# Performance work log

Measured on AMD Instinct MI355X. Metric: run time of the kernel, lower is better.

Reference implementation:

```python
import jax, jax.numpy as jnp
import numpy as np

IGNORE_INDEX = -100
BETA = 0.1
B, T, H, V = 4, 512, 4096, 32000

def setup_inputs() -> dict:
    key = jax.random.key(0)
    ks = jax.random.split(key, 8)
    s = 1.0 / np.sqrt(H)
    return {
        "_input": jax.random.normal(ks[0], (B, T, H), jnp.float32),
        "weight": jax.random.normal(ks[1], (V, H), jnp.float32) * s,
        "bias": jax.random.normal(ks[2], (V,), jnp.float32) * 0.01,
        "target": jax.random.randint(ks[3], (B, T), 0, V, jnp.int64),
        "preference_labels": jax.random.bernoulli(ks[4], 0.5, (B,)),
        "ref_input": jax.random.normal(ks[5], (B, T, H), jnp.float32),
        "ref_weight": jax.random.normal(ks[6], (V, H), jnp.float32) * s,
        "ref_bias": jax.random.normal(ks[7], (V,), jnp.float32) * 0.01,
        "kl": jax.random.uniform(jax.random.fold_in(key, 9), (1,), jnp.float32),
    }

def _avg_log_prob(x, w, b, target):
    # logits: [B, T, V]
    logits = jnp.einsum("bth,vh->btv", x, w) + b
    lse = jax.nn.logsumexp(logits, axis=-1)            # [B, T]
    idx = jnp.clip(target, 0, None)[..., None]
    tgt_logit = jnp.take_along_axis(logits, idx, axis=-1)[..., 0]
    per_tok_logp = tgt_logit - lse                     # [B, T]
    mask = (target != IGNORE_INDEX).astype(per_tok_logp.dtype)
    denom = jnp.maximum(mask.sum(-1), 1.0)
    return (per_tok_logp * mask).sum(-1) / denom       # [B]

def reference(_input, weight, bias, target, preference_labels, ref_input, ref_weight, ref_bias, kl):
    avg_logp = _avg_log_prob(_input, weight, bias, target)
    ref_avg_logp = jax.lax.stop_gradient(_avg_log_prob(ref_input, ref_weight, ref_bias, target))
    logratios = avg_logp - ref_avg_logp                # [B]
    multiplier = jnp.where(preference_labels, 1.0, -1.0)
    losses = 1.0 - jax.nn.sigmoid(BETA * (logratios - kl[0]) * multiplier)
    return losses.sum() / target.shape[0]
```

## Files before the change

### kernel.cpp

```cpp
#include <hip/hip_runtime.h>
#include <hip/hip_bf16.h>
#include <stdint.h>

#define HD 4096
#define VD 32000
#define BT 2048
#define TT 512
#define IGNORE_IDX (-100)

#define BM 256
#define BN 256
#define BKT 64
#define KT (HD / BKT)
#define NB (VD / BN)
#define MB (BT / BM)
#define NWG2 (MB * NB * 2)

#define NCHUNK (VD / 64)

typedef __attribute__((ext_vector_type(8))) short short8;
typedef __attribute__((ext_vector_type(4))) float f32x4;

__device__ __forceinline__ uint16_t f2bf(float f) {
    uint32_t u = __float_as_uint(f);
    u += 0x7FFFu + ((u >> 16) & 1u);
    return (uint16_t)(u >> 16);
}

__device__ __forceinline__ void gload16(const void* g, void* l) {
    __builtin_amdgcn_global_load_lds(
        (const __attribute__((address_space(1))) void*)g,
        (__attribute__((address_space(3))) void*)l, 16, 0, 0);
}

#define SBAR __builtin_amdgcn_sched_barrier(0)

__global__ void convert_x(const float* __restrict__ x0, const float* __restrict__ x1,
                          uint16_t* __restrict__ xbf) {
    const int64_t n4 = (int64_t)BT * HD / 4;
    ushort4* o0 = (ushort4*)xbf;
    ushort4* o1 = (ushort4*)(xbf + (int64_t)BT * HD);
    for (int64_t i = blockIdx.x * (int64_t)blockDim.x + threadIdx.x; i < n4;
         i += (int64_t)gridDim.x * blockDim.x) {
        float4 a = ((const float4*)x0)[i];
        float4 b = ((const float4*)x1)[i];
        ushort4 ua, ub;
        ua.x = f2bf(a.x); ua.y = f2bf(a.y); ua.z = f2bf(a.z); ua.w = f2bf(a.w);
        ub.x = f2bf(b.x); ub.y = f2bf(b.y); ub.z = f2bf(b.z); ub.w = f2bf(b.w);
        o0[i] = ua;
        o1[i] = ub;
    }
}

__global__ void convert_w(const float* __restrict__ w0, const float* __restrict__ w1,
                          uint16_t* __restrict__ wbf) {
    const int64_t n4 = (int64_t)VD * HD / 4;
    ushort4* o0 = (ushort4*)wbf;
    ushort4* o1 = (ushort4*)(wbf + (int64_t)VD * HD);
    for (int64_t i = blockIdx.x * (int64_t)blockDim.x + threadIdx.x; i < n4;
         i += (int64_t)gridDim.x * blockDim.x) {
        float4 a = ((const float4*)w0)[i];
        float4 b = ((const float4*)w1)[i];
        ushort4 ua, ub;
        ua.x = f2bf(a.x); ua.y = f2bf(a.y); ua.z = f2bf(a.z); ua.w = f2bf(a.w);
        ub.x = f2bf(b.x); ub.y = f2bf(b.y); ub.z = f2bf(b.z); ub.w = f2bf(b.w);
        o0[i] = ua;
        o1[i] = ub;
    }
}

__device__ __forceinline__ void mfma16(
    const short8& a0k0, const short8& a0k1, const short8& a1k0, const short8& a1k1,
    const short8 (&bfr)[4][2], f32x4* acc0, f32x4* acc1)
{
    __builtin_amdgcn_s_setprio(1);
#pragma unroll
    for (int ni = 0; ni < 4; ++ni)
        acc0[ni] = __builtin_amdgcn_mfma_f32_16x16x32_bf16(a0k0, bfr[ni][0], acc0[ni], 0, 0, 0);
#pragma unroll
    for (int ni = 0; ni < 4; ++ni)
        acc1[ni] = __builtin_amdgcn_mfma_f32_16x16x32_bf16(a1k0, bfr[ni][0], acc1[ni], 0, 0, 0);
#pragma unroll
    for (int ni = 0; ni < 4; ++ni)
        acc0[ni] = __builtin_amdgcn_mfma_f32_16x16x32_bf16(a0k1, bfr[ni][1], acc0[ni], 0, 0, 0);
#pragma unroll
    for (int ni = 0; ni < 4; ++ni)
        acc1[ni] = __builtin_amdgcn_mfma_f32_16x16x32_bf16(a1k1, bfr[ni][1], acc1[ni], 0, 0, 0);
    __builtin_amdgcn_s_setprio(0);
}

template<int CUR>
__device__ __forceinline__ void tile_body(
    int t,
    const uint16_t* __restrict__ agp, const uint16_t* __restrict__ bgp,
    char* aLdst, char* bLdst,
    const char* pA0, const char* pA1, const char* pB0, const char* pB1,
    f32x4 (&acc)[8][4])
{
    constexpr int CB  = CUR * 32768;
    constexpr int NXB = (CUR ^ 1) * 32768;
    const bool more = (t + 1) < KT;
    const int ko = (t + 1) * BKT;

    short8 bfr[4][2];
    short8 af0k0, af0k1, af1k0, af1k1;

#define BARR do { SBAR; __builtin_amdgcn_s_barrier(); SBAR; } while (0)
#define LOAD_AF(mi0)                                                   \
    af0k0 = *(const short8*)(pA0 + (mi0) * 2048 + CB);                 \
    af0k1 = *(const short8*)(pA1 + (mi0) * 2048 + CB);                 \
    af1k0 = *(const short8*)(pA0 + ((mi0) + 1) * 2048 + CB);           \
    af1k1 = *(const short8*)(pA1 + ((mi0) + 1) * 2048 + CB);

#pragma unroll
    for (int ni = 0; ni < 4; ++ni) {
        bfr[ni][0] = *(const short8*)(pB0 + ni * 2048 + CB);
        bfr[ni][1] = *(const short8*)(pB1 + ni * 2048 + CB);
    }
    LOAD_AF(0);
    if (more) {
        gload16(bgp + (size_t)(0 * 32) * HD + ko, bLdst + NXB + 0 * 4096);
        gload16(bgp + (size_t)(1 * 32) * HD + ko, bLdst + NXB + 1 * 4096);
    }
    BARR;
    mfma16(af0k0, af0k1, af1k0, af1k1, bfr, acc[0], acc[1]);
    BARR;

    LOAD_AF(2);
    if (more) {
        gload16(bgp + (size_t)(2 * 32) * HD + ko, bLdst + NXB + 2 * 4096);
        gload16(bgp + (size_t)(3 * 32) * HD + ko, bLdst + NXB + 3 * 4096);
    }
    BARR;
    mfma16(af0k0, af0k1, af1k0, af1k1, bfr, acc[2], acc[3]);
    SBAR; asm volatile("s_waitcnt vmcnt(4)" ::: "memory"); SBAR;
    BARR;

    LOAD_AF(4);
    if (more) {
        gload16(agp + (size_t)(0 * 32) * HD + ko, aLdst + NXB + 0 * 4096);
        gload16(agp + (size_t)(1 * 32) * HD + ko, aLdst + NXB + 1 * 4096);
    }
    BARR;
    mfma16(af0k0, af0k1, af1k0, af1k1, bfr, acc[4], acc[5]);
    BARR;

    LOAD_AF(6);
    if (more) {
        gload16(agp + (size_t)(2 * 32) * HD + ko, aLdst + NXB + 2 * 4096);
        gload16(agp + (size_t)(3 * 32) * HD + ko, aLdst + NXB + 3 * 4096);
    }
    BARR;
    mfma16(af0k0, af0k1, af1k0, af1k1, bfr, acc[6], acc[7]);
    SBAR;
    if (more) { asm volatile("s_waitcnt vmcnt(2)" ::: "memory"); }
    else      { asm volatile("s_waitcnt vmcnt(0)" ::: "memory"); }
    SBAR;
    BARR;
#undef LOAD_AF
#undef BARR
}

__global__ __launch_bounds__(512, 2) void gemm_lse_bf(
    const uint16_t* __restrict__ xbf, const uint16_t* __restrict__ wbf,
    const float* __restrict__ b0, const float* __restrict__ b1,
    const int* __restrict__ target,
    float* __restrict__ partials, float* __restrict__ tgtlog)
{
    __shared__ uint16_t As[2 * BM * BKT];
    __shared__ uint16_t Bs[2 * BN * BKT];

    const int orig = blockIdx.x;
    const int wgid = (orig & 7) * (NWG2 / 8) + (orig >> 3);
    const int mb    = wgid & 7;
    const int rest  = wgid >> 3;
    const int nb    = rest % NB;
    const int model = rest / NB;

    const uint16_t* xb = xbf + (size_t)model * BT * HD;
    const uint16_t* wb = wbf + (size_t)model * VD * HD;
    const float* bias  = model ? b1 : b0;

    const int row0 = mb * BM;
    const int c0   = nb * BN;

    const int tid    = threadIdx.x;
    const int lane   = tid & 63;
    const int wid    = tid >> 6;
    const int wr     = wid >> 2;
    const int wc     = wid & 3;

    const int lane15 = lane & 15;
    const int kg     = lane >> 4;
    const int swz    = (lane & 7) << 4;

    const int srow8 = lane >> 3;
    const int slot  = (lane & 7) ^ srow8;
    const uint16_t* agp = xb + (size_t)(row0 + wr * 128 + wc * 8 + srow8) * HD + slot * 8;
    const int bq = wr * 2 + (wc & 1);
    const uint16_t* bgp = wb + (size_t)(c0 + (wc >> 1) * 128 + bq * 8 + srow8) * HD + slot * 8;
    char* aLdst = (char*)As + wr * 16384 + wc * 1024;
    char* bLdst = (char*)Bs + (wc >> 1) * 16384 + bq * 1024;

    const int arow_b = wr * 128 + lane15;
    const int brow_b = wc * 64 + lane15;
    const char* pA0 = (const char*)As + ((arow_b * 128 + 0  + kg * 16) ^ swz);
    const char* pA1 = (const char*)As + ((arow_b * 128 + 64 + kg * 16) ^ swz);
    const char* pB0 = (const char*)Bs + ((brow_b * 128 + 0  + kg * 16) ^ swz);
    const char* pB1 = (const char*)Bs + ((brow_b * 128 + 64 + kg * 16) ^ swz);

    f32x4 acc[8][4];
#pragma unroll
    for (int i = 0; i < 8; ++i)
#pragma unroll
        for (int j = 0; j < 4; ++j) acc[i][j] = (f32x4){0.f, 0.f, 0.f, 0.f};

#pragma unroll
    for (int j = 0; j < 4; ++j)
        gload16(bgp + (size_t)(j * 32) * HD, bLdst + j * 4096);
#pragma unroll
    for (int j = 0; j < 4; ++j)
        gload16(agp + (size_t)(j * 32) * HD, aLdst + j * 4096);
    SBAR; asm volatile("s_waitcnt vmcnt(0)" ::: "memory"); SBAR;
    __builtin_amdgcn_s_barrier();
    SBAR;

    for (int t2 = 0; t2 < KT; t2 += 2) {
        tile_body<0>(t2,     agp, bgp, aLdst, bLdst, pA0, pA1, pB0, pB1, acc);
        tile_body<1>(t2 + 1, agp, bgp, aLdst, bLdst, pA0, pA1, pB0, pB1, acc);
    }

    float bv4[4];
#pragma unroll
    for (int ni = 0; ni < 4; ++ni) bv4[ni] = bias[c0 + wc * 64 + ni * 16 + lane15];

#pragma unroll
    for (int mi = 0; mi < 8; ++mi) {
        const int grow_base = row0 + wr * 128 + mi * 16 + kg * 4;
#pragma unroll
        for (int j = 0; j < 4; ++j) {
            const int grow = grow_base + j;
            float v[4];
#pragma unroll
            for (int ni = 0; ni < 4; ++ni) v[ni] = acc[mi][ni][j] + bv4[ni];
            float m = fmaxf(fmaxf(v[0], v[1]), fmaxf(v[2], v[3]));
#pragma unroll
            for (int msk = 1; msk < 16; msk <<= 1)
                m = fmaxf(m, __shfl_xor(m, msk));
            float s = __expf(v[0] - m) + __expf(v[1] - m) +
                      __expf(v[2] - m) + __expf(v[3] - m);
#pragma unroll
            for (int msk = 1; msk < 16; msk <<= 1)
                s += __shfl_xor(s, msk);
            const int tg = target[grow];
#pragma unroll
            for (int ni = 0; ni < 4; ++ni) {
                const int gcol = c0 + wc * 64 + ni * 16 + lane15;
                if (tg == gcol) tgtlog[model * BT + grow] = v[ni];
            }
            if (lane15 == 0) {
                const size_t po = ((size_t)(model * BT + grow) * NCHUNK + nb * 4 + wc) * 2;
                partials[po]     = m;
                partials[po + 1] = s;
            }
        }
    }
}

__global__ __launch_bounds__(256) void gemm_lse_f32(
    const uint16_t* __restrict__ xbf,
    const float* __restrict__ w0, const float* __restrict__ b0,
    const float* __restrict__ w1, const float* __restrict__ b1,
    const int* __restrict__ target,
    float* __restrict__ partials, float* __restrict__ tgtlog)
{
    const int orig = blockIdx.x;
    const int wgid = (orig & 7) * 1000 + (orig >> 3);
    const int mb    = wgid & 7;
    const int rest  = wgid >> 3;
    const int chunk = rest % 500;
    const int model = rest / 500;

    const float* w    = model ? w1 : w0;
    const float* bias = model ? b1 : b0;
    const uint16_t* xb = xbf + (size_t)model * BT * HD;

    const int row0 = mb * 256;
    const int c0   = chunk * 64;

    const int tid  = threadIdx.x;
    const int lane = tid & 63;
    const int wid  = tid >> 6;

    __shared__ uint16_t As_[256 * 64];
    __shared__ uint16_t Bs_[64 * 64];

    f32x4 acc[4][4];
#pragma unroll
    for (int i = 0; i < 4; ++i)
#pragma unroll
        for (int j = 0; j < 4; ++j) acc[i][j] = (f32x4){0.f, 0.f, 0.f, 0.f};

    const int srow8 = lane >> 3;
    const int slot  = (lane & 7) ^ srow8;
    const uint16_t* agsrc = xb + (size_t)(row0 + wid * 64 + srow8) * HD + slot * 8;
    char* aldst = (char*)As_ + wid * 8192;

    const int ss   = tid & 7;
    const int srow = tid >> 3;
    const int swz_w = (srow & 7) << 4;
    const float* bptr = w + (size_t)(c0 + srow) * HD + ss * 8;

    const int lane15 = lane & 15;
    const int kg     = lane >> 4;
    const int swz_r  = (lane & 7) << 4;

    for (int kt = 0; kt < 64; ++kt) {
        const int kofs = kt * 64;
#pragma unroll
        for (int c = 0; c < 8; ++c)
            gload16(agsrc + (size_t)c * 8 * HD + kofs, aldst + c * 1024);
        {
            float4 bv[2][2];
#pragma unroll
            for (int r = 0; r < 2; ++r) {
                const float* p = bptr + (size_t)r * 32 * HD + kofs;
                bv[r][0] = *(const float4*)(p);
                bv[r][1] = *(const float4*)(p + 4);
            }
#pragma unroll
            for (int r = 0; r < 2; ++r) {
                const int row_l = srow + r * 32;
                float fv[8] = {bv[r][0].x, bv[r][0].y, bv[r][0].z, bv[r][0].w,
                               bv[r][1].x, bv[r][1].y, bv[r][1].z, bv[r][1].w};
                uint32_t pk[4];
#pragma unroll
                for (int e = 0; e < 4; ++e)
                    pk[e] = (uint32_t)f2bf(fv[2 * e]) | ((uint32_t)f2bf(fv[2 * e + 1]) << 16);
                const int off = (row_l * 128 + ss * 16) ^ swz_w;
                *(uint4*)((char*)Bs_ + off) = *(uint4*)pk;
            }
        }
        __syncthreads();
#pragma unroll
        for (int ks = 0; ks < 2; ++ks) {
            short8 af[4], bf[4];
#pragma unroll
            for (int mi = 0; mi < 4; ++mi) {
                const int arow = wid * 64 + mi * 16 + lane15;
                const int off = (arow * 128 + ks * 64 + kg * 16) ^ swz_r;
                af[mi] = *(const short8*)((const char*)As_ + off);
            }
#pragma unroll
            for (int ni = 0; ni < 4; ++ni) {
                const int brow = ni * 16 + lane15;
                const int off = (brow * 128 + ks * 64 + kg * 16) ^ swz_r;
                bf[ni] = *(const short8*)((const char*)Bs_ + off);
            }
#pragma unroll
            for (int mi = 0; mi < 4; ++mi)
#pragma unroll
                for (int ni = 0; ni < 4; ++ni)
                    acc[mi][ni] = __builtin_amdgcn_mfma_f32_16x16x32_bf16(
                        af[mi], bf[ni], acc[mi][ni], 0, 0, 0);
        }
        __syncthreads();
    }

    float bv4[4];
#pragma unroll
    for (int ni = 0; ni < 4; ++ni) bv4[ni] = bias[c0 + ni * 16 + lane15];

#pragma unroll
    for (int mi = 0; mi < 4; ++mi) {
        const int grow_base = row0 + wid * 64 + mi * 16 + kg * 4;
#pragma unroll
        for (int j = 0; j < 4; ++j) {
            const int grow = grow_base + j;
            float v[4];
#pragma unroll
            for (int ni = 0; ni < 4; ++ni) v[ni] = acc[mi][ni][j] + bv4[ni];
            float m = fmaxf(fmaxf(v[0], v[1]), fmaxf(v[2], v[3]));
#pragma unroll
            for (int msk = 1; msk < 16; msk <<= 1)
                m = fmaxf(m, __shfl_xor(m, msk));
            float s = __expf(v[0] - m) + __expf(v[1] - m) +
                      __expf(v[2] - m) + __expf(v[3] - m);
#pragma unroll
            for (int msk = 1; msk < 16; msk <<= 1)
                s += __shfl_xor(s, msk);
            const int tg = target[grow];
#pragma unroll
            for (int ni = 0; ni < 4; ++ni) {
                const int gcol = c0 + ni * 16 + lane15;
                if (tg == gcol) tgtlog[model * BT + grow] = v[ni];
            }
            if (lane15 == 0) {
                const size_t po = ((size_t)(model * BT + grow) * NCHUNK + chunk) * 2;
                partials[po]     = m;
                partials[po + 1] = s;
            }
        }
    }
}

__global__ void lse_reduce(const float* __restrict__ partials,
                           const float* __restrict__ tgtlog,
                           float* __restrict__ logp) {
    const int gw = blockIdx.x * (blockDim.x >> 6) + (threadIdx.x >> 6);
    if (gw >= 2 * BT) return;
    const int lane = threadIdx.x & 63;
    const float* p = partials + (size_t)gw * NCHUNK * 2;

    float m = -1e30f;
#pragma unroll
    for (int i = 0; i < 8; ++i) {
        const int c = lane + i * 64;
        if (c < NCHUNK) m = fmaxf(m, p[c * 2]);
    }
#pragma unroll
    for (int msk = 1; msk < 64; msk <<= 1) m = fmaxf(m, __shfl_xor(m, msk));
    float s = 0.f;
#pragma unroll
    for (int i = 0; i < 8; ++i) {
        const int c = lane + i * 64;
        if (c < NCHUNK) s += p[c * 2 + 1] * __expf(p[c * 2] - m);
    }
#pragma unroll
    for (int msk = 1; msk < 64; msk <<= 1) s += __shfl_xor(s, msk);
    if (lane == 0) {
        const float lse = m + __logf(s);
        logp[gw] = tgtlog[gw] - lse;
    }
}

__global__ void final_loss(const float* __restrict__ logp, const int* __restrict__ target,
                           const int* __restrict__ pref, const float* __restrict__ kl,
                           float* __restrict__ out) {
    const int t = threadIdx.x;
    const int lane = t & 63, wv = t >> 6;
    __shared__ float rp[4][8], rr[4][8], rm[4][8];
#pragma unroll
    for (int b = 0; b < 4; ++b) {
        const int idx = b * TT + t;
        const int tg = target[idx];
        const bool mk = (tg != IGNORE_IDX);
        float lp = mk ? logp[idx] : 0.f;
        float lr = mk ? logp[BT + idx] : 0.f;
        float mc = mk ? 1.f : 0.f;
        for (int off = 32; off; off >>= 1) {
            lp += __shfl_down(lp, off);
            lr += __shfl_down(lr, off);
            mc += __shfl_down(mc, off);
        }
        if (lane == 0) { rp[b][wv] = lp; rr[b][wv] = lr; rm[b][wv] = mc; }
    }
    __syncthreads();
    if (t == 0) {
        float loss = 0.f;
        for (int b = 0; b < 4; ++b) {
            float sp = 0.f, sr = 0.f, sm = 0.f;
            for (int i = 0; i < 8; ++i) { sp += rp[b][i]; sr += rr[b][i]; sm += rm[b][i]; }
            const float denom = fmaxf(sm, 1.f);
            const float lrb = (sp - sr) / denom;
            const float mult = pref[b] ? 1.f : -1.f;
            const float z = 0.1f * (lrb - kl[0]) * mult;
            loss += 1.f / (1.f + __expf(z));
        }
        out[0] = loss * 0.25f;
    }
}

extern "C" void kernel_launch(void* const* d_in, const int* in_sizes, int n_in,
                              void* d_out, int out_size, void* d_ws, size_t ws_size,
                              hipStream_t stream) {
    const float* x    = (const float*)d_in[0];
    const float* w0   = (const float*)d_in[1];
    const float* b0   = (const float*)d_in[2];
    const int*   tgt  = (const int*)d_in[3];
    const int*   pref = (const int*)d_in[4];
    const float* xr   = (const float*)d_in[5];
    const float* w1   = (const float*)d_in[6];
    const float* b1   = (const float*)d_in[7];
    const float* kl   = (const float*)d_in[8];
    float* out = (float*)d_out;

    const size_t xbf_b  = (size_t)2 * BT * HD * 2;
    const size_t part_b = (size_t)2 * BT * NCHUNK * 2 * 4;
    const size_t tl_b   = (size_t)2 * BT * 4;
    const size_t wbf_b  = (size_t)2 * VD * HD * 2;

    char* wp = (char*)d_ws;
    uint16_t* xbf     = (uint16_t*)wp;                 wp += xbf_b;
    float*    partials = (float*)wp;                   wp += part_b;
    float*    tgtlog   = (float*)wp;                   wp += tl_b;
    float*    logp     = (float*)wp;                   wp += tl_b;
    uint16_t* wbf      = (uint16_t*)wp;
    const bool use_wbf = ws_size >= (xbf_b + part_b + 2 * tl_b + wbf_b);

    hipLaunchKernelGGL(convert_x, dim3(1024), dim3(256), 0, stream, x, xr, xbf);
    if (use_wbf) {
        hipLaunchKernelGGL(convert_w, dim3(4096), dim3(256), 0, stream, w0, w1, wbf);
        hipLaunchKernelGGL(gemm_lse_bf, dim3(NWG2), dim3(512), 0, stream,
                           xbf, wbf, b0, b1, tgt, partials, tgtlog);
    } else {
        hipLaunchKernelGGL(gemm_lse_f32, dim3(8000), dim3(256), 0, stream,
                           xbf, w0, b0, w1, b1, tgt, partials, tgtlog);
    }
    hipLaunchKernelGGL(lse_reduce, dim3(2 * BT / 4), dim3(256), 0, stream,
                       partials, tgtlog, logp);
    hipLaunchKernelGGL(final_loss, dim3(1), dim3(512), 0, stream, logp, tgt, pref, kl, out);
}
```

Measured before the change: 1.291 ms.

## Switch bf16 GEMM to 32x32x16 MFMA with restructured LDS reads and prefetch

Replaces the 16x16x32 bf16 MFMA tiling with 32x32x16 MFMA instructions. Each wave now holds a 4x2 grid of 16-float accumulators, and LDS fragments are read per k-slice with a matching XOR swizzle. All eight next-tile global-to-LDS loads are issued at the start of the first phase, with one full vmcnt wait at the end of each tile. The aim is fewer MFMA and LDS read instructions per flop and fewer split waits. The cost is an epilogue with 32-lane shuffle reductions and a larger per-instruction accumulator footprint.

```diff
diff --git a/kernel.cpp b/kernel.cpp
--- a/kernel.cpp
+++ b/kernel.cpp
@@ -20,6 +20,7 @@
 
 typedef __attribute__((ext_vector_type(8))) short short8;
 typedef __attribute__((ext_vector_type(4))) float f32x4;
+typedef __attribute__((ext_vector_type(16))) float f32x16;
 
 __device__ __forceinline__ uint16_t f2bf(float f) {
     uint32_t u = __float_as_uint(f);
@@ -69,95 +70,64 @@
     }
 }
 
-__device__ __forceinline__ void mfma16(
-    const short8& a0k0, const short8& a0k1, const short8& a1k0, const short8& a1k1,
-    const short8 (&bfr)[4][2], f32x4* acc0, f32x4* acc1)
-{
-    __builtin_amdgcn_s_setprio(1);
-#pragma unroll
-    for (int ni = 0; ni < 4; ++ni)
-        acc0[ni] = __builtin_amdgcn_mfma_f32_16x16x32_bf16(a0k0, bfr[ni][0], acc0[ni], 0, 0, 0);
-#pragma unroll
-    for (int ni = 0; ni < 4; ++ni)
-        acc1[ni] = __builtin_amdgcn_mfma_f32_16x16x32_bf16(a1k0, bfr[ni][0], acc1[ni], 0, 0, 0);
-#pragma unroll
-    for (int ni = 0; ni < 4; ++ni)
-        acc0[ni] = __builtin_amdgcn_mfma_f32_16x16x32_bf16(a0k1, bfr[ni][1], acc0[ni], 0, 0, 0);
-#pragma unroll
-    for (int ni = 0; ni < 4; ++ni)
-        acc1[ni] = __builtin_amdgcn_mfma_f32_16x16x32_bf16(a1k1, bfr[ni][1], acc1[ni], 0, 0, 0);
-    __builtin_amdgcn_s_setprio(0);
-}
+#define MFMA32(a, b, c) __builtin_amdgcn_mfma_f32_32x32x16_bf16(a, b, c, 0, 0, 0)
 
 template<int CUR>
 __device__ __forceinline__ void tile_body(
     int t,
     const uint16_t* __restrict__ agp, const uint16_t* __restrict__ bgp,
     char* aLdst, char* bLdst,
-    const char* pA0, const char* pA1, const char* pB0, const char* pB1,
-    f32x4 (&acc)[8][4])
+    const char* pAk0, const char* pAk1, const char* pAk2, const char* pAk3,
+    const char* pBk0, const char* pBk1, const char* pBk2, const char* pBk3,
+    f32x16 (&acc)[4][2])
 {
     constexpr int CB  = CUR * 32768;
     constexpr int NXB = (CUR ^ 1) * 32768;
     const bool more = (t + 1) < KT;
     const int ko = (t + 1) * BKT;
 
-    short8 bfr[4][2];
-    short8 af0k0, af0k1, af1k0, af1k1;
-
 #define BARR do { SBAR; __builtin_amdgcn_s_barrier(); SBAR; } while (0)
-#define LOAD_AF(mi0)                                                   \
-    af0k0 = *(const short8*)(pA0 + (mi0) * 2048 + CB);                 \
-    af0k1 = *(const short8*)(pA1 + (mi0) * 2048 + CB);                 \
-    af1k0 = *(const short8*)(pA0 + ((mi0) + 1) * 2048 + CB);           \
-    af1k1 = *(const short8*)(pA1 + ((mi0) + 1) * 2048 + CB);
-
-#pragma unroll
-    for (int ni = 0; ni < 4; ++ni) {
-        bfr[ni][0] = *(const short8*)(pB0 + ni * 2048 + CB);
-        bfr[ni][1] = *(const short8*)(pB1 + ni * 2048 + CB);
-    }
-    LOAD_AF(0);
-    if (more) {
-        gload16(bgp + (size_t)(0 * 32) * HD + ko, bLdst + NXB + 0 * 4096);
-        gload16(bgp + (size_t)(1 * 32) * HD + ko, bLdst + NXB + 1 * 4096);
-    }
+#define PHASE(PA, PB, STG) do {                                        \
+    short8 a0 = *(const short8*)(PA + 0 * 4096 + CB);                  \
+    short8 a1 = *(const short8*)(PA + 1 * 4096 + CB);                  \
+    short8 a2 = *(const short8*)(PA + 2 * 4096 + CB);                  \
+    short8 a3 = *(const short8*)(PA + 3 * 4096 + CB);                  \
+    short8 b0 = *(const short8*)(PB + 0 * 4096 + CB);                  \
+    short8 b1 = *(const short8*)(PB + 1 * 4096 + CB);                  \
+    STG                                                                \
+    __builtin_amdgcn_s_setprio(1);                                     \
+    acc[0][0] = MFMA32(a0, b0, acc[0][0]);                             \
+    acc[1][0] = MFMA32(a1, b0, acc[1][0]);                             \
+    acc[2][0] = MFMA32(a2, b0, acc[2][0]);                             \
+    acc[3][0] = MFMA32(a3, b0, acc[3][0]);                             \
+    acc[0][1] = MFMA32(a0, b1, acc[0][1]);                             \
+    acc[1][1] = MFMA32(a1, b1, acc[1][1]);                             \
+    acc[2][1] = MFMA32(a2, b1, acc[2][1]);                             \
+    acc[3][1] = MFMA32(a3, b1, acc[3][1]);                             \
+    __builtin_amdgcn_s_setprio(0);                                     \
+} while (0)
+
+    PHASE(pAk0, pBk0,
+        if (more) {
+            gload16(bgp + (size_t)(0 * 32) * HD + ko, bLdst + NXB + 0 * 4096);
+            gload16(bgp + (size_t)(1 * 32) * HD + ko, bLdst + NXB + 1 * 4096);
+            gload16(bgp + (size_t)(2 * 32) * HD + ko, bLdst + NXB + 2 * 4096);
+            gload16(bgp + (size_t)(3 * 32) * HD + ko, bLdst + NXB + 3 * 4096);
+            gload16(agp + (size_t)(0 * 32) * HD + ko, aLdst + NXB + 0 * 4096);
+            gload16(agp + (size_t)(1 * 32) * HD + ko, aLdst + NXB + 1 * 4096);
+            gload16(agp + (size_t)(2 * 32) * HD + ko, aLdst + NXB + 2 * 4096);
+            gload16(agp + (size_t)(3 * 32) * HD + ko, aLdst + NXB + 3 * 4096);
+        });
     BARR;
-    mfma16(af0k0, af0k1, af1k0, af1k1, bfr, acc[0], acc[1]);
+    PHASE(pAk1, pBk1, ;);
     BARR;
-
-    LOAD_AF(2);
-    if (more) {
-        gload16(bgp + (size_t)(2 * 32) * HD + ko, bLdst + NXB + 2 * 4096);
-        gload16(bgp + (size_t)(3 * 32) * HD + ko, bLdst + NXB + 3 * 4096);
-    }
+    PHASE(pAk2, pBk2, ;);
     BARR;
-    mfma16(af0k0, af0k1, af1k0, af1k1, bfr, acc[2], acc[3]);
-    SBAR; asm volatile("s_waitcnt vmcnt(4)" ::: "memory"); SBAR;
-    BARR;
-
-    LOAD_AF(4);
-    if (more) {
-        gload16(agp + (size_t)(0 * 32) * HD + ko, aLdst + NXB + 0 * 4096);
-        gload16(agp + (size_t)(1 * 32) * HD + ko, aLdst + NXB + 1 * 4096);
-    }
-    BARR;
-    mfma16(af0k0, af0k1, af1k0, af1k1, bfr, acc[4], acc[5]);
-    BARR;
-
-    LOAD_AF(6);
-    if (more) {
-        gload16(agp + (size_t)(2 * 32) * HD + ko, aLdst + NXB + 2 * 4096);
-        gload16(agp + (size_t)(3 * 32) * HD + ko, aLdst + NXB + 3 * 4096);
-    }
-    BARR;
-    mfma16(af0k0, af0k1, af1k0, af1k1, bfr, acc[6], acc[7]);
+    PHASE(pAk3, pBk3, ;);
+    SBAR; asm volatile("s_waitcnt vmcnt(0)" ::: "memory"); SBAR;
+    __builtin_amdgcn_s_barrier();
     SBAR;
-    if (more) { asm volatile("s_waitcnt vmcnt(2)" ::: "memory"); }
-    else      { asm volatile("s_waitcnt vmcnt(0)" ::: "memory"); }
-    SBAR;
-    BARR;
-#undef LOAD_AF
+#undef PHASE
 #undef BARR
 }
 
@@ -190,9 +160,8 @@
     const int wr     = wid >> 2;
     const int wc     = wid & 3;
 
-    const int lane15 = lane & 15;
-    const int kg     = lane >> 4;
-    const int swz    = (lane & 7) << 4;
+    const int l31 = lane & 31;
+    const int hi  = lane >> 5;
 
     const int srow8 = lane >> 3;
     const int slot  = (lane & 7) ^ srow8;
@@ -202,18 +171,26 @@
     char* aLdst = (char*)As + wr * 16384 + wc * 1024;
     char* bLdst = (char*)Bs + (wc >> 1) * 16384 + bq * 1024;
 
-    const int arow_b = wr * 128 + lane15;
-    const int brow_b = wc * 64 + lane15;
-    const char* pA0 = (const char*)As + ((arow_b * 128 + 0  + kg * 16) ^ swz);
-    const char* pA1 = (const char*)As + ((arow_b * 128 + 64 + kg * 16) ^ swz);
-    const char* pB0 = (const char*)Bs + ((brow_b * 128 + 0  + kg * 16) ^ swz);
-    const char* pB1 = (const char*)Bs + ((brow_b * 128 + 64 + kg * 16) ^ swz);
-
-    f32x4 acc[8][4];
-#pragma unroll
-    for (int i = 0; i < 8; ++i)
-#pragma unroll
-        for (int j = 0; j < 4; ++j) acc[i][j] = (f32x4){0.f, 0.f, 0.f, 0.f};
+    const int row_a = wr * 128 + l31;
+    const int row_b = wc * 64 + l31;
+    const int r7a = row_a & 7;
+    const int r7b = row_b & 7;
+    const char* pAk0 = (const char*)As + row_a * 128 + (((0 * 2 + hi) ^ r7a) << 4);
+    const char* pAk1 = (const char*)As + row_a * 128 + (((1 * 2 + hi) ^ r7a) << 4);
+    const char* pAk2 = (const char*)As + row_a * 128 + (((2 * 2 + hi) ^ r7a) << 4);
+    const char* pAk3 = (const char*)As + row_a * 128 + (((3 * 2 + hi) ^ r7a) << 4);
+    const char* pBk0 = (const char*)Bs + row_b * 128 + (((0 * 2 + hi) ^ r7b) << 4);
+    const char* pBk1 = (const char*)Bs + row_b * 128 + (((1 * 2 + hi) ^ r7b) << 4);
+    const char* pBk2 = (const char*)Bs + row_b * 128 + (((2 * 2 + hi) ^ r7b) << 4);
+    const char* pBk3 = (const char*)Bs + row_b * 128 + (((3 * 2 + hi) ^ r7b) << 4);
+
+    f32x16 acc[4][2];
+#pragma unroll
+    for (int i = 0; i < 4; ++i)
+#pragma unroll
+        for (int j = 0; j < 2; ++j)
+#pragma unroll
+            for (int e = 0; e < 16; ++e) acc[i][j][e] = 0.f;
 
 #pragma unroll
     for (int j = 0; j < 4; ++j)
@@ -226,39 +203,36 @@
     SBAR;
 
     for (int t2 = 0; t2 < KT; t2 += 2) {
-        tile_body<0>(t2,     agp, bgp, aLdst, bLdst, pA0, pA1, pB0, pB1, acc);
-        tile_body<1>(t2 + 1, agp, bgp, aLdst, bLdst, pA0, pA1, pB0, pB1, acc);
-    }
-
-    float bv4[4];
-#pragma unroll
-    for (int ni = 0; ni < 4; ++ni) bv4[ni] = bias[c0 + wc * 64 + ni * 16 + lane15];
-
-#pragma unroll
-    for (int mi = 0; mi < 8; ++mi) {
-        const int grow_base = row0 + wr * 128 + mi * 16 + kg * 4;
-#pragma unroll
-        for (int j = 0; j < 4; ++j) {
-            const int grow = grow_base + j;
-            float v[4];
-#pragma unroll
-            for (int ni = 0; ni < 4; ++ni) v[ni] = acc[mi][ni][j] + bv4[ni];
-            float m = fmaxf(fmaxf(v[0], v[1]), fmaxf(v[2], v[3]));
-#pragma unroll
-            for (int msk = 1; msk < 16; msk <<= 1)
+        tile_body<0>(t2,     agp, bgp, aLdst, bLdst,
+                     pAk0, pAk1, pAk2, pAk3, pBk0, pBk1, pBk2, pBk3, acc);
+        tile_body<1>(t2 + 1, agp, bgp, aLdst, bLdst,
+                     pAk0, pAk1, pAk2, pAk3, pBk0, pBk1, pBk2, pBk3, acc);
+    }
+
+    const float bv0 = bias[c0 + wc * 64 + l31];
+    const float bv1 = bias[c0 + wc * 64 + 32 + l31];
+    const int col0 = c0 + wc * 64 + l31;
+
+#pragma unroll
+    for (int rf = 0; rf < 4; ++rf) {
+#pragma unroll
+        for (int r = 0; r < 16; ++r) {
+            const int rowl = (r & 3) + 8 * (r >> 2) + 4 * hi;
+            const int grow = row0 + wr * 128 + rf * 32 + rowl;
+            const float v0 = acc[rf][0][r] + bv0;
+            const float v1 = acc[rf][1][r] + bv1;
+            float m = fmaxf(v0, v1);
+#pragma unroll
+            for (int msk = 1; msk < 32; msk <<= 1)
                 m = fmaxf(m, __shfl_xor(m, msk));
-            float s = __expf(v[0] - m) + __expf(v[1] - m) +
-                      __expf(v[2] - m) + __expf(v[3] - m);
-#pragma unroll
-            for (int msk = 1; msk < 16; msk <<= 1)
+            float s = __expf(v0 - m) + __expf(v1 - m);
+#pragma unroll
+            for (int msk = 1; msk < 32; msk <<= 1)
                 s += __shfl_xor(s, msk);
             const int tg = target[grow];
-#pragma unroll
-            for (int ni = 0; ni < 4; ++ni) {
-                const int gcol = c0 + wc * 64 + ni * 16 + lane15;
-                if (tg == gcol) tgtlog[model * BT + grow] = v[ni];
-            }
-            if (lane15 == 0) {
+            if (tg == col0)      tgtlog[model * BT + grow] = v0;
+            if (tg == col0 + 32) tgtlog[model * BT + grow] = v1;
+            if (l31 == 0) {
                 const size_t po = ((size_t)(model * BT + grow) * NCHUNK + nb * 4 + wc) * 2;
                 partials[po]     = m;
                 partials[po + 1] = s;
```

After: 1.584 ms. 1.23x slower.

## Issue all next-tile global loads upfront and use a single barrier per K-tile

Applied to the files above, without the earlier changes.

Replaces the four-phase interleaved schedule, with barriers between each MFMA group and staggered global-to-LDS loads, with one up-front burst of all eight async global loads for the next tile. All MFMA groups then run back to back, followed by one vmcnt(0) wait and one workgroup barrier. This cuts barrier count per K-step from about eight to one. It gives up the fine-grained wave interleaving and staggered memory issue, so global-load latency may be less well hidden and LDS read contention across waves may change.

```diff
diff --git a/kernel.cpp b/kernel.cpp
--- a/kernel.cpp
+++ b/kernel.cpp
@@ -102,63 +102,36 @@
     const bool more = (t + 1) < KT;
     const int ko = (t + 1) * BKT;
 
+    if (more) {
+#pragma unroll
+        for (int j = 0; j < 4; ++j)
+            gload16(bgp + (size_t)(j * 32) * HD + ko, bLdst + NXB + j * 4096);
+#pragma unroll
+        for (int j = 0; j < 4; ++j)
+            gload16(agp + (size_t)(j * 32) * HD + ko, aLdst + NXB + j * 4096);
+    }
+    SBAR;
+
     short8 bfr[4][2];
-    short8 af0k0, af0k1, af1k0, af1k1;
-
-#define BARR do { SBAR; __builtin_amdgcn_s_barrier(); SBAR; } while (0)
-#define LOAD_AF(mi0)                                                   \
-    af0k0 = *(const short8*)(pA0 + (mi0) * 2048 + CB);                 \
-    af0k1 = *(const short8*)(pA1 + (mi0) * 2048 + CB);                 \
-    af1k0 = *(const short8*)(pA0 + ((mi0) + 1) * 2048 + CB);           \
-    af1k1 = *(const short8*)(pA1 + ((mi0) + 1) * 2048 + CB);
-
 #pragma unroll
     for (int ni = 0; ni < 4; ++ni) {
         bfr[ni][0] = *(const short8*)(pB0 + ni * 2048 + CB);
         bfr[ni][1] = *(const short8*)(pB1 + ni * 2048 + CB);
     }
-    LOAD_AF(0);
-    if (more) {
-        gload16(bgp + (size_t)(0 * 32) * HD + ko, bLdst + NXB + 0 * 4096);
-        gload16(bgp + (size_t)(1 * 32) * HD + ko, bLdst + NXB + 1 * 4096);
-    }
-    BARR;
-    mfma16(af0k0, af0k1, af1k0, af1k1, bfr, acc[0], acc[1]);
-    BARR;
-
-    LOAD_AF(2);
-    if (more) {
-        gload16(bgp + (size_t)(2 * 32) * HD + ko, bLdst + NXB + 2 * 4096);
-        gload16(bgp + (size_t)(3 * 32) * HD + ko, bLdst + NXB + 3 * 4096);
-    }
-    BARR;
-    mfma16(af0k0, af0k1, af1k0, af1k1, bfr, acc[2], acc[3]);
-    SBAR; asm volatile("s_waitcnt vmcnt(4)" ::: "memory"); SBAR;
-    BARR;
-
-    LOAD_AF(4);
-    if (more) {
-        gload16(agp + (size_t)(0 * 32) * HD + ko, aLdst + NXB + 0 * 4096);
-        gload16(agp + (size_t)(1 * 32) * HD + ko, aLdst + NXB + 1 * 4096);
-    }
-    BARR;
-    mfma16(af0k0, af0k1, af1k0, af1k1, bfr, acc[4], acc[5]);
-    BARR;
-
-    LOAD_AF(6);
-    if (more) {
-        gload16(agp + (size_t)(2 * 32) * HD + ko, aLdst + NXB + 2 * 4096);
-        gload16(agp + (size_t)(3 * 32) * HD + ko, aLdst + NXB + 3 * 4096);
-    }
-    BARR;
-    mfma16(af0k0, af0k1, af1k0, af1k1, bfr, acc[6], acc[7]);
+#pragma unroll
+    for (int p = 0; p < 4; ++p) {
+        const short8 a0 = *(const short8*)(pA0 + (2 * p) * 2048 + CB);
+        const short8 a1 = *(const short8*)(pA1 + (2 * p) * 2048 + CB);
+        const short8 a2 = *(const short8*)(pA0 + (2 * p + 1) * 2048 + CB);
+        const short8 a3 = *(const short8*)(pA1 + (2 * p + 1) * 2048 + CB);
+        mfma16(a0, a1, a2, a3, bfr, acc[2 * p], acc[2 * p + 1]);
+    }
+
     SBAR;
-    if (more) { asm volatile("s_waitcnt vmcnt(2)" ::: "memory"); }
-    else      { asm volatile("s_waitcnt vmcnt(0)" ::: "memory"); }
+    asm volatile("s_waitcnt vmcnt(0)" ::: "memory");
     SBAR;
-    BARR;
-#undef LOAD_AF
-#undef BARR
+    __builtin_amdgcn_s_barrier();
+    SBAR;
 }
 
 __global__ __launch_bounds__(512, 2) void gemm_lse_bf(
```

New measurement: 1.505 ms. +16.5%, slower.

## Switch GEMM+LSE path from bf16 to scaled fp8 MFMA with fp8 conversion

Applied to the files above, without the earlier changes.

Inputs and weights are now converted to fp8 (weights pre-scaled by 64, with the offset undone through the MFMA scale exponent) instead of bf16. The main GEMM uses the 16x16x128 scaled f8f6f4 MFMA with a 128-byte K tile and a reworked LDS swizzle. The aim is to double matrix throughput and halve conversion-output and operand traffic. The cost is much lower numerical precision in the logits, which may break tolerance on the log-prob differences.

```diff
diff --git a/kernel.cpp b/kernel.cpp
--- a/kernel.cpp
+++ b/kernel.cpp
@@ -10,8 +10,8 @@
 
 #define BM 256
 #define BN 256
-#define BKT 64
-#define KT (HD / BKT)
+#define BKT8 128
+#define KT8 (HD / BKT8)
 #define NB (VD / BN)
 #define MB (BT / BM)
 #define NWG2 (MB * NB * 2)
@@ -20,6 +20,7 @@
 
 typedef __attribute__((ext_vector_type(8))) short short8;
 typedef __attribute__((ext_vector_type(4))) float f32x4;
+typedef __attribute__((ext_vector_type(8))) int i32x8;
 
 __device__ __forceinline__ uint16_t f2bf(float f) {
     uint32_t u = __float_as_uint(f);
@@ -34,6 +35,255 @@
 }
 
 #define SBAR __builtin_amdgcn_sched_barrier(0)
+
+__global__ void convert_x_fp8(const float* __restrict__ x0, const float* __restrict__ x1,
+                              uint8_t* __restrict__ xq) {
+    const int64_t n8 = (int64_t)BT * HD / 8;
+    uint2* o0 = (uint2*)xq;
+    uint2* o1 = (uint2*)(xq + (size_t)BT * HD);
+    for (int64_t i = blockIdx.x * (int64_t)blockDim.x + threadIdx.x; i < n8;
+         i += (int64_t)gridDim.x * blockDim.x) {
+        float4 a = ((const float4*)x0)[2 * i];
+        float4 b = ((const float4*)x0)[2 * i + 1];
+        int lo = __builtin_amdgcn_cvt_pk_fp8_f32(a.x, a.y, 0, false);
+        lo     = __builtin_amdgcn_cvt_pk_fp8_f32(a.z, a.w, lo, true);
+        int hi = __builtin_amdgcn_cvt_pk_fp8_f32(b.x, b.y, 0, false);
+        hi     = __builtin_amdgcn_cvt_pk_fp8_f32(b.z, b.w, hi, true);
+        o0[i] = make_uint2((unsigned)lo, (unsigned)hi);
+        a = ((const float4*)x1)[2 * i];
+        b = ((const float4*)x1)[2 * i + 1];
+        lo = __builtin_amdgcn_cvt_pk_fp8_f32(a.x, a.y, 0, false);
+        lo = __builtin_amdgcn_cvt_pk_fp8_f32(a.z, a.w, lo, true);
+        hi = __builtin_amdgcn_cvt_pk_fp8_f32(b.x, b.y, 0, false);
+        hi = __builtin_amdgcn_cvt_pk_fp8_f32(b.z, b.w, hi, true);
+        o1[i] = make_uint2((unsigned)lo, (unsigned)hi);
+    }
+}
+
+__global__ void convert_w_fp8(const float* __restrict__ w0, const float* __restrict__ w1,
+                              uint8_t* __restrict__ wq) {
+    const int64_t n8 = (int64_t)VD * HD / 8;
+    uint2* o0 = (uint2*)wq;
+    uint2* o1 = (uint2*)(wq + (size_t)VD * HD);
+    for (int64_t i = blockIdx.x * (int64_t)blockDim.x + threadIdx.x; i < n8;
+         i += (int64_t)gridDim.x * blockDim.x) {
+        float4 a = ((const float4*)w0)[2 * i];
+        float4 b = ((const float4*)w0)[2 * i + 1];
+        int lo = __builtin_amdgcn_cvt_pk_fp8_f32(a.x * 64.f, a.y * 64.f, 0, false);
+        lo     = __builtin_amdgcn_cvt_pk_fp8_f32(a.z * 64.f, a.w * 64.f, lo, true);
+        int hi = __builtin_amdgcn_cvt_pk_fp8_f32(b.x * 64.f, b.y * 64.f, 0, false);
+        hi     = __builtin_amdgcn_cvt_pk_fp8_f32(b.z * 64.f, b.w * 64.f, hi, true);
+        o0[i] = make_uint2((unsigned)lo, (unsigned)hi);
+        a = ((const float4*)w1)[2 * i];
+        b = ((const float4*)w1)[2 * i + 1];
+        lo = __builtin_amdgcn_cvt_pk_fp8_f32(a.x * 64.f, a.y * 64.f, 0, false);
+        lo = __builtin_amdgcn_cvt_pk_fp8_f32(a.z * 64.f, a.w * 64.f, lo, true);
+        hi = __builtin_amdgcn_cvt_pk_fp8_f32(b.x * 64.f, b.y * 64.f, 0, false);
+        hi = __builtin_amdgcn_cvt_pk_fp8_f32(b.z * 64.f, b.w * 64.f, hi, true);
+        o1[i] = make_uint2((unsigned)lo, (unsigned)hi);
+    }
+}
+
+__device__ __forceinline__ i32x8 ld_frag(const char* pe, const char* po, int off) {
+    uint4 lo = *(const uint4*)(pe + off);
+    uint4 hi = *(const uint4*)(po + off);
+    i32x8 r;
+    r[0] = lo.x; r[1] = lo.y; r[2] = lo.z; r[3] = lo.w;
+    r[4] = hi.x; r[5] = hi.y; r[6] = hi.z; r[7] = hi.w;
+    return r;
+}
+
+__device__ __forceinline__ void mfma8(
+    const i32x8& a0, const i32x8& a1, const i32x8 (&bfr)[4],
+    f32x4* acc0, f32x4* acc1)
+{
+    __builtin_amdgcn_s_setprio(1);
+#pragma unroll
+    for (int ni = 0; ni < 4; ++ni)
+        acc0[ni] = __builtin_amdgcn_mfma_scale_f32_16x16x128_f8f6f4(
+            a0, bfr[ni], acc0[ni], 0, 0, 0, 127, 0, 121);
+#pragma unroll
+    for (int ni = 0; ni < 4; ++ni)
+        acc1[ni] = __builtin_amdgcn_mfma_scale_f32_16x16x128_f8f6f4(
+            a1, bfr[ni], acc1[ni], 0, 0, 0, 127, 0, 121);
+    __builtin_amdgcn_s_setprio(0);
+}
+
+template<int CUR>
+__device__ __forceinline__ void tile8_body(
+    int t,
+    const uint8_t* __restrict__ agp, const uint8_t* __restrict__ bgp,
+    char* aLdst, char* bLdst,
+    const char* pAe, const char* pAo, const char* pBe, const char* pBo,
+    f32x4 (&acc)[8][4])
+{
+    constexpr int CB  = CUR * 32768;
+    constexpr int NXB = (CUR ^ 1) * 32768;
+    const bool more = (t + 1) < KT8;
+    const int ko = (t + 1) * BKT8;
+
+    i32x8 bfr[4];
+    i32x8 a0, a1;
+
+#define BARR do { SBAR; __builtin_amdgcn_s_barrier(); SBAR; } while (0)
+
+#pragma unroll
+    for (int ni = 0; ni < 4; ++ni)
+        bfr[ni] = ld_frag(pBe, pBo, ni * 2048 + CB);
+    a0 = ld_frag(pAe, pAo, 0 * 2048 + CB);
+    a1 = ld_frag(pAe, pAo, 1 * 2048 + CB);
+    if (more) {
+        gload16(bgp + (size_t)(0 * 32) * HD + ko, bLdst + NXB + 0 * 4096);
+        gload16(bgp + (size_t)(1 * 32) * HD + ko, bLdst + NXB + 1 * 4096);
+    }
+    BARR;
+    mfma8(a0, a1, bfr, acc[0], acc[1]);
+    BARR;
+
+    a0 = ld_frag(pAe, pAo, 2 * 2048 + CB);
+    a1 = ld_frag(pAe, pAo, 3 * 2048 + CB);
+    if (more) {
+        gload16(bgp + (size_t)(2 * 32) * HD + ko, bLdst + NXB + 2 * 4096);
+        gload16(bgp + (size_t)(3 * 32) * HD + ko, bLdst + NXB + 3 * 4096);
+    }
+    BARR;
+    mfma8(a0, a1, bfr, acc[2], acc[3]);
+    SBAR;
+    if (more) { asm volatile("s_waitcnt vmcnt(4)" ::: "memory"); }
+    else      { asm volatile("s_waitcnt vmcnt(0)" ::: "memory"); }
+    SBAR;
+    BARR;
+
+    a0 = ld_frag(pAe, pAo, 4 * 2048 + CB);
+    a1 = ld_frag(pAe, pAo, 5 * 2048 + CB);
+    if (more) {
+        gload16(agp + (size_t)(0 * 32) * HD + ko, aLdst + NXB + 0 * 4096);
+        gload16(agp + (size_t)(1 * 32) * HD + ko, aLdst + NXB + 1 * 4096);
+    }
+    BARR;
+    mfma8(a0, a1, bfr, acc[4], acc[5]);
+    BARR;
+
+    a0 = ld_frag(pAe, pAo, 6 * 2048 + CB);
+    a1 = ld_frag(pAe, pAo, 7 * 2048 + CB);
+    if (more) {
+        gload16(agp + (size_t)(2 * 32) * HD + ko, aLdst + NXB + 2 * 4096);
+        gload16(agp + (size_t)(3 * 32) * HD + ko, aLdst + NXB + 3 * 4096);
+    }
+    BARR;
+    mfma8(a0, a1, bfr, acc[6], acc[7]);
+    SBAR;
+    if (more) { asm volatile("s_waitcnt vmcnt(2)" ::: "memory"); }
+    else      { asm volatile("s_waitcnt vmcnt(0)" ::: "memory"); }
+    SBAR;
+    BARR;
+#undef BARR
+}
+
+__global__ __launch_bounds__(512, 2) void gemm_lse_fp8(
+    const uint8_t* __restrict__ xq, const uint8_t* __restrict__ wq,
+    const float* __restrict__ b0, const float* __restrict__ b1,
+    const int* __restrict__ target,
+    float* __restrict__ partials, float* __restrict__ tgtlog)
+{
+    __shared__ uint8_t As[2 * BM * BKT8];
+    __shared__ uint8_t Bs[2 * BN * BKT8];
+
+    const int orig = blockIdx.x;
+    const int wgid = (orig & 7) * (NWG2 / 8) + (orig >> 3);
+    const int mb    = wgid & 7;
+    const int rest  = wgid >> 3;
+    const int nb    = rest % NB;
+    const int model = rest / NB;
+
+    const uint8_t* xb = xq + (size_t)model * BT * HD;
+    const uint8_t* wb = wq + (size_t)model * VD * HD;
+    const float* bias = model ? b1 : b0;
+
+    const int row0 = mb * BM;
+    const int c0   = nb * BN;
+
+    const int tid    = threadIdx.x;
+    const int lane   = tid & 63;
+    const int wid    = tid >> 6;
+    const int wr     = wid >> 2;
+    const int wc     = wid & 3;
+
+    const int lane15 = lane & 15;
+    const int kg     = lane >> 4;
+
+    const int srow8 = lane >> 3;
+    const int slot  = (lane & 7) ^ srow8;
+    const uint8_t* agp = xb + (size_t)(row0 + wr * 128 + wc * 8 + srow8) * HD + slot * 16;
+    const int bq = wr * 2 + (wc & 1);
+    const uint8_t* bgp = wb + (size_t)(c0 + (wc >> 1) * 128 + bq * 8 + srow8) * HD + slot * 16;
+    char* aLdst = (char*)As + wr * 16384 + wc * 1024;
+    char* bLdst = (char*)Bs + (wc >> 1) * 16384 + bq * 1024;
+
+    const int row_a = wr * 128 + lane15;
+    const int row_b = wc * 64 + lane15;
+    const char* pAe = (const char*)As + row_a * 128 + ((( 2 * kg    ) ^ (row_a & 7)) << 4);
+    const char* pAo = (const char*)As + row_a * 128 + (((2 * kg + 1) ^ (row_a & 7)) << 4);
+    const char* pBe = (const char*)Bs + row_b * 128 + ((( 2 * kg    ) ^ (row_b & 7)) << 4);
+    const char* pBo = (const char*)Bs + row_b * 128 + (((2 * kg + 1) ^ (row_b & 7)) << 4);
+
+    f32x4 acc[8][4];
+#pragma unroll
+    for (int i = 0; i < 8; ++i)
+#pragma unroll
+        for (int j = 0; j < 4; ++j) acc[i][j] = (f32x4){0.f, 0.f, 0.f, 0.f};
+
+#pragma unroll
+    for (int j = 0; j < 4; ++j)
+        gload16(bgp + (size_t)(j * 32) * HD, bLdst + j * 4096);
+#pragma unroll
+    for (int j = 0; j < 4; ++j)
+        gload16(agp + (size_t)(j * 32) * HD, aLdst + j * 4096);
+    SBAR; asm volatile("s_waitcnt vmcnt(0)" ::: "memory"); SBAR;
+    __builtin_amdgcn_s_barrier();
+    SBAR;
+
+    for (int t2 = 0; t2 < KT8; t2 += 2) {
+        tile8_body<0>(t2,     agp, bgp, aLdst, bLdst, pAe, pAo, pBe, pBo, acc);
+        tile8_body<1>(t2 + 1, agp, bgp, aLdst, bLdst, pAe, pAo, pBe, pBo, acc);
+    }
+
+    float bv4[4];
+#pragma unroll
+    for (int ni = 0; ni < 4; ++ni) bv4[ni] = bias[c0 + wc * 64 + ni * 16 + lane15];
+
+#pragma unroll
+    for (int mi = 0; mi < 8; ++mi) {
+        const int grow_base = row0 + wr * 128 + mi * 16 + kg * 4;
+#pragma unroll
+        for (int j = 0; j < 4; ++j) {
+            const int grow = grow_base + j;
+            float v[4];
+#pragma unroll
+            for (int ni = 0; ni < 4; ++ni) v[ni] = acc[mi][ni][j] + bv4[ni];
+            float m = fmaxf(fmaxf(v[0], v[1]), fmaxf(v[2], v[3]));
+#pragma unroll
+            for (int msk = 1; msk < 16; msk <<= 1)
+                m = fmaxf(m, __shfl_xor(m, msk));
+            float s = __expf(v[0] - m) + __expf(v[1] - m) +
+                      __expf(v[2] - m) + __expf(v[3] - m);
+#pragma unroll
+            for (int msk = 1; msk < 16; msk <<= 1)
+                s += __shfl_xor(s, msk);
+            const int tg = target[grow];
+#pragma unroll
+            for (int ni = 0; ni < 4; ++ni) {
+                const int gcol = c0 + wc * 64 + ni * 16 + lane15;
+                if (tg == gcol) tgtlog[model * BT + grow] = v[ni];
+            }
+            if (lane15 == 0) {
+                const size_t po = ((size_t)(model * BT + grow) * NCHUNK + nb * 4 + wc) * 2;
+                partials[po]     = m;
+                partials[po + 1] = s;
+            }
+        }
+    }
+}
 
 __global__ void convert_x(const float* __restrict__ x0, const float* __restrict__ x1,
                           uint16_t* __restrict__ xbf) {
@@ -52,221 +302,6 @@
     }
 }
 
-__global__ void convert_w(const float* __restrict__ w0, const float* __restrict__ w1,
-                          uint16_t* __restrict__ wbf) {
-    const int64_t n4 = (int64_t)VD * HD / 4;
-    ushort4* o0 = (ushort4*)wbf;
-    ushort4* o1 = (ushort4*)(wbf + (int64_t)VD * HD);
-    for (int64_t i = blockIdx.x * (int64_t)blockDim.x + threadIdx.x; i < n4;
-         i += (int64_t)gridDim.x * blockDim.x) {
-        float4 a = ((const float4*)w0)[i];
-        float4 b = ((const float4*)w1)[i];
-        ushort4 ua, ub;
-        ua.x = f2bf(a.x); ua.y = f2bf(a.y); ua.z = f2bf(a.z); ua.w = f2bf(a.w);
-        ub.x = f2bf(b.x); ub.y = f2bf(b.y); ub.z = f2bf(b.z); ub.w = f2bf(b.w);
-        o0[i] = ua;
-        o1[i] = ub;
-    }
-}
-
-__device__ __forceinline__ void mfma16(
-    const short8& a0k0, const short8& a0k1, const short8& a1k0, const short8& a1k1,
-    const short8 (&bfr)[4][2], f32x4* acc0, f32x4* acc1)
-{
-    __builtin_amdgcn_s_setprio(1);
-#pragma unroll
-    for (int ni = 0; ni < 4; ++ni)
-        acc0[ni] = __builtin_amdgcn_mfma_f32_16x16x32_bf16(a0k0, bfr[ni][0], acc0[ni], 0, 0, 0);
-#pragma unroll
-    for (int ni = 0; ni < 4; ++ni)
-        acc1[ni] = __builtin_amdgcn_mfma_f32_16x16x32_bf16(a1k0, bfr[ni][0], acc1[ni], 0, 0, 0);
-#pragma unroll
-    for (int ni = 0; ni < 4; ++ni)
-        acc0[ni] = __builtin_amdgcn_mfma_f32_16x16x32_bf16(a0k1, bfr[ni][1], acc0[ni], 0, 0, 0);
-#pragma unroll
-    for (int ni = 0; ni < 4; ++ni)
-        acc1[ni] = __builtin_amdgcn_mfma_f32_16x16x32_bf16(a1k1, bfr[ni][1], acc1[ni], 0, 0, 0);
-    __builtin_amdgcn_s_setprio(0);
-}
-
-template<int CUR>
-__device__ __forceinline__ void tile_body(
-    int t,
-    const uint16_t* __restrict__ agp, const uint16_t* __restrict__ bgp,
-    char* aLdst, char* bLdst,
-    const char* pA0, const char* pA1, const char* pB0, const char* pB1,
-    f32x4 (&acc)[8][4])
-{
-    constexpr int CB  = CUR * 32768;
-    constexpr int NXB = (CUR ^ 1) * 32768;
-    const bool more = (t + 1) < KT;
-    const int ko = (t + 1) * BKT;
-
-    short8 bfr[4][2];
-    short8 af0k0, af0k1, af1k0, af1k1;
-
-#define BARR do { SBAR; __builtin_amdgcn_s_barrier(); SBAR; } while (0)
-#define LOAD_AF(mi0)                                                   \
-    af0k0 = *(const short8*)(pA0 + (mi0) * 2048 + CB);                 \
-    af0k1 = *(const short8*)(pA1 + (mi0) * 2048 + CB);                 \
-    af1k0 = *(const short8*)(pA0 + ((mi0) + 1) * 2048 + CB);           \
-    af1k1 = *(const short8*)(pA1 + ((mi0) + 1) * 2048 + CB);
-
-#pragma unroll
-    for (int ni = 0; ni < 4; ++ni) {
-        bfr[ni][0] = *(const short8*)(pB0 + ni * 2048 + CB);
-        bfr[ni][1] = *(const short8*)(pB1 + ni * 2048 + CB);
-    }
-    LOAD_AF(0);
-    if (more) {
-        gload16(bgp + (size_t)(0 * 32) * HD + ko, bLdst + NXB + 0 * 4096);
-        gload16(bgp + (size_t)(1 * 32) * HD + ko, bLdst + NXB + 1 * 4096);
-    }
-    BARR;
-    mfma16(af0k0, af0k1, af1k0, af1k1, bfr, acc[0], acc[1]);
-    BARR;
-
-    LOAD_AF(2);
-    if (more) {
-        gload16(bgp + (size_t)(2 * 32) * HD + ko, bLdst + NXB + 2 * 4096);
-        gload16(bgp + (size_t)(3 * 32) * HD + ko, bLdst + NXB + 3 * 4096);
-    }
-    BARR;
-    mfma16(af0k0, af0k1, af1k0, af1k1, bfr, acc[2], acc[3]);
-    SBAR; asm volatile("s_waitcnt vmcnt(4)" ::: "memory"); SBAR;
-    BARR;
-
-    LOAD_AF(4);
-    if (more) {
-        gload16(agp + (size_t)(0 * 32) * HD + ko, aLdst + NXB + 0 * 4096);
-        gload16(agp + (size_t)(1 * 32) * HD + ko, aLdst + NXB + 1 * 4096);
-    }
-    BARR;
-    mfma16(af0k0, af0k1, af1k0, af1k1, bfr, acc[4], acc[5]);
-    BARR;
-
-    LOAD_AF(6);
-    if (more) {
-        gload16(agp + (size_t)(2 * 32) * HD + ko, aLdst + NXB + 2 * 4096);
-        gload16(agp + (size_t)(3 * 32) * HD + ko, aLdst + NXB + 3 * 4096);
-    }
-    BARR;
-    mfma16(af0k0, af0k1, af1k0, af1k1, bfr, acc[6], acc[7]);
-    SBAR;
-    if (more) { asm volatile("s_waitcnt vmcnt(2)" ::: "memory"); }
-    else      { asm volatile("s_waitcnt vmcnt(0)" ::: "memory"); }
-    SBAR;
-    BARR;
-#undef LOAD_AF
-#undef BARR
-}
-
-__global__ __launch_bounds__(512, 2) void gemm_lse_bf(
-    const uint16_t* __restrict__ xbf, const uint16_t* __restrict__ wbf,
-    const float* __restrict__ b0, const float* __restrict__ b1,
-    const int* __restrict__ target,
-    float* __restrict__ partials, float* __restrict__ tgtlog)
-{
-    __shared__ uint16_t As[2 * BM * BKT];
-    __shared__ uint16_t Bs[2 * BN * BKT];
-
-    const int orig = blockIdx.x;
-    const int wgid = (orig & 7) * (NWG2 / 8) + (orig >> 3);
-    const int mb    = wgid & 7;
-    const int rest  = wgid >> 3;
-    const int nb    = rest % NB;
-    const int model = rest / NB;
-
-    const uint16_t* xb = xbf + (size_t)model * BT * HD;
-    const uint16_t* wb = wbf + (size_t)model * VD * HD;
-    const float* bias  = model ? b1 : b0;
-
-    const int row0 = mb * BM;
-    const int c0   = nb * BN;
-
-    const int tid    = threadIdx.x;
-    const int lane   = tid & 63;
-    const int wid    = tid >> 6;
-    const int wr     = wid >> 2;
-    const int wc     = wid & 3;
-
-    const int lane15 = lane & 15;
-    const int kg     = lane >> 4;
-    const int swz    = (lane & 7) << 4;
-
-    const int srow8 = lane >> 3;
-    const int slot  = (lane & 7) ^ srow8;
-    const uint16_t* agp = xb + (size_t)(row0 + wr * 128 + wc * 8 + srow8) * HD + slot * 8;
-    const int bq = wr * 2 + (wc & 1);
-    const uint16_t* bgp = wb + (size_t)(c0 + (wc >> 1) * 128 + bq * 8 + srow8) * HD + slot * 8;
-    char* aLdst = (char*)As + wr * 16384 + wc * 1024;
-    char* bLdst = (char*)Bs + (wc >> 1) * 16384 + bq * 1024;
-
-    const int arow_b = wr * 128 + lane15;
-    const int brow_b = wc * 64 + lane15;
-    const char* pA0 = (const char*)As + ((arow_b * 128 + 0  + kg * 16) ^ swz);
-    const char* pA1 = (const char*)As + ((arow_b * 128 + 64 + kg * 16) ^ swz);
-    const char* pB0 = (const char*)Bs + ((brow_b * 128 + 0  + kg * 16) ^ swz);
-    const char* pB1 = (const char*)Bs + ((brow_b * 128 + 64 + kg * 16) ^ swz);
-
-    f32x4 acc[8][4];
-#pragma unroll
-    for (int i = 0; i < 8; ++i)
-#pragma unroll
-        for (int j = 0; j < 4; ++j) acc[i][j] = (f32x4){0.f, 0.f, 0.f, 0.f};
-
-#pragma unroll
-    for (int j = 0; j < 4; ++j)
-        gload16(bgp + (size_t)(j * 32) * HD, bLdst + j * 4096);
-#pragma unroll
-    for (int j = 0; j < 4; ++j)
-        gload16(agp + (size_t)(j * 32) * HD, aLdst + j * 4096);
-    SBAR; asm volatile("s_waitcnt vmcnt(0)" ::: "memory"); SBAR;
-    __builtin_amdgcn_s_barrier();
-    SBAR;
-
-    for (int t2 = 0; t2 < KT; t2 += 2) {
-        tile_body<0>(t2,     agp, bgp, aLdst, bLdst, pA0, pA1, pB0, pB1, acc);
-        tile_body<1>(t2 + 1, agp, bgp, aLdst, bLdst, pA0, pA1, pB0, pB1, acc);
-    }
-
-    float bv4[4];
-#pragma unroll
-    for (int ni = 0; ni < 4; ++ni) bv4[ni] = bias[c0 + wc * 64 + ni * 16 + lane15];
-
-#pragma unroll
-    for (int mi = 0; mi < 8; ++mi) {
-        const int grow_base = row0 + wr * 128 + mi * 16 + kg * 4;
-#pragma unroll
-        for (int j = 0; j < 4; ++j) {
-            const int grow = grow_base + j;
-            float v[4];
-#pragma unroll
-            for (int ni = 0; ni < 4; ++ni) v[ni] = acc[mi][ni][j] + bv4[ni];
-            float m = fmaxf(fmaxf(v[0], v[1]), fmaxf(v[2], v[3]));
-#pragma unroll
-            for (int msk = 1; msk < 16; msk <<= 1)
-                m = fmaxf(m, __shfl_xor(m, msk));
-            float s = __expf(v[0] - m) + __expf(v[1] - m) +
-                      __expf(v[2] - m) + __expf(v[3] - m);
-#pragma unroll
-            for (int msk = 1; msk < 16; msk <<= 1)
-                s += __shfl_xor(s, msk);
-            const int tg = target[grow];
-#pragma unroll
-            for (int ni = 0; ni < 4; ++ni) {
-                const int gcol = c0 + wc * 64 + ni * 16 + lane15;
-                if (tg == gcol) tgtlog[model * BT + grow] = v[ni];
-            }
-            if (lane15 == 0) {
-                const size_t po = ((size_t)(model * BT + grow) * NCHUNK + nb * 4 + wc) * 2;
-                partials[po]     = m;
-                partials[po + 1] = s;
-            }
-        }
-    }
-}
-
 __global__ __launch_bounds__(256) void gemm_lse_f32(
     const uint16_t* __restrict__ xbf,
     const float* __restrict__ w0, const float* __restrict__ b0,
@@ -485,25 +520,28 @@
     const float* kl   = (const float*)d_in[8];
     float* out = (float*)d_out;
 
-    const size_t xbf_b  = (size_t)2 * BT * HD * 2;
     const size_t part_b = (size_t)2 * BT * NCHUNK * 2 * 4;
     const size_t tl_b   = (size_t)2 * BT * 4;
-    const size_t wbf_b  = (size_t)2 * VD * HD * 2;
+    const size_t xq_b   = (size_t)2 * BT * HD;
+    const size_t wq_b   = (size_t)2 * VD * HD;
 
     char* wp = (char*)d_ws;
-    uint16_t* xbf     = (uint16_t*)wp;                 wp += xbf_b;
-    float*    partials = (float*)wp;                   wp += part_b;
-    float*    tgtlog   = (float*)wp;                   wp += tl_b;
-    float*    logp     = (float*)wp;                   wp += tl_b;
-    uint16_t* wbf      = (uint16_t*)wp;
-    const bool use_wbf = ws_size >= (xbf_b + part_b + 2 * tl_b + wbf_b);
-
-    hipLaunchKernelGGL(convert_x, dim3(1024), dim3(256), 0, stream, x, xr, xbf);
-    if (use_wbf) {
-        hipLaunchKernelGGL(convert_w, dim3(4096), dim3(256), 0, stream, w0, w1, wbf);
-        hipLaunchKernelGGL(gemm_lse_bf, dim3(NWG2), dim3(512), 0, stream,
-                           xbf, wbf, b0, b1, tgt, partials, tgtlog);
+    float*   partials = (float*)wp;                  wp += part_b;
+    float*   tgtlog   = (float*)wp;                  wp += tl_b;
+    float*   logp     = (float*)wp;                  wp += tl_b;
+    uint8_t* xq       = (uint8_t*)wp;
+    uint8_t* wq       = xq + xq_b;
+    uint16_t* xbf     = (uint16_t*)wp;
+
+    const bool use_fp8 = ws_size >= (part_b + 2 * tl_b + xq_b + wq_b);
+
+    if (use_fp8) {
+        hipLaunchKernelGGL(convert_x_fp8, dim3(512), dim3(256), 0, stream, x, xr, xq);
+        hipLaunchKernelGGL(convert_w_fp8, dim3(4096), dim3(256), 0, stream, w0, w1, wq);
+        hipLaunchKernelGGL(gemm_lse_fp8, dim3(NWG2), dim3(512), 0, stream,
+                           xq, wq, b0, b1, tgt, partials, tgtlog);
     } else {
+        hipLaunchKernelGGL(convert_x, dim3(1024), dim3(256), 0, stream, x, xr, xbf);
         hipLaunchKernelGGL(gemm_lse_f32, dim3(8000), dim3(256), 0, stream,
                            xbf, w0, b0, w1, b1, tgt, partials, tgtlog);
     }
```

Result: slower. 2.727 ms (+111.2%).
